# Kernel optimization log

Hardware: AMD Instinct MI355X
Metric: run time of the kernel (lower is better)

## Reference

```python
import jax, jax.numpy as jnp
import numpy as np

D, H, DK, DFF = 256, 8, 32, 1024
EPS = 1e-5

def _layernorm(x, g, b):
    mu = jnp.mean(x, axis=-1, keepdims=True)
    var = jnp.mean((x - mu) ** 2, axis=-1, keepdims=True)
    return (x - mu) * jax.lax.rsqrt(var + EPS) * g + b

def setup_inputs() -> dict:
    key = jax.random.key(0)
    ks = jax.random.split(key, 16)
    s = 1.0 / np.sqrt(D)
    sf = 1.0 / np.sqrt(DFF)
    return {
        "src": jax.random.normal(ks[0], (2, 4096, D), jnp.float32),
        "Wq": jax.random.uniform(ks[1], (H, D, DK), jnp.float32, -s, s),
        "bq": jax.random.uniform(ks[2], (H, DK), jnp.float32, -s, s),
        "Wk": jax.random.uniform(ks[3], (H, D, DK), jnp.float32, -s, s),
        "bk": jax.random.uniform(ks[4], (H, DK), jnp.float32, -s, s),
        "Wv": jax.random.uniform(ks[5], (H, D, DK), jnp.float32, -s, s),
        "bv": jax.random.uniform(ks[6], (H, DK), jnp.float32, -s, s),
        "Wo": jax.random.uniform(ks[7], (H * DK, D), jnp.float32, -s, s),
        "bo": jax.random.uniform(ks[8], (D,), jnp.float32, -s, s),
        "ln1_g": jnp.ones((D,), jnp.float32),
        "ln1_b": jnp.zeros((D,), jnp.float32),
        "W1": jax.random.uniform(ks[9], (D, DFF), jnp.float32, -s, s),
        "b1": jax.random.uniform(ks[10], (DFF,), jnp.float32, -s, s),
        "W2": jax.random.uniform(ks[11], (DFF, D), jnp.float32, -sf, sf),
        "b2": jax.random.uniform(ks[12], (D,), jnp.float32, -sf, sf),
        "ln2_g": jnp.ones((D,), jnp.float32),
        "ln2_b": jnp.zeros((D,), jnp.float32),
    }

def reference(src, Wq, bq, Wk, bk, Wv, bv, Wo, bo, ln1_g, ln1_b, W1, b1, W2, b2, ln2_g, ln2_b):
    B, S, _ = src.shape
    # per-head projections, batched over heads: [B,H,S,DK]
    q = jnp.einsum("bsd,hdk->bhsk", src, Wq) + bq[None, :, None, :]
    k = jnp.einsum("bsd,hdk->bhsk", src, Wk) + bk[None, :, None, :]
    v = jnp.einsum("bsd,hdk->bhsk", src, Wv) + bv[None, :, None, :]
    scale = jnp.sqrt(jnp.asarray(DK, src.dtype))
    scores = jnp.einsum("bhsk,bhtk->bhst", q, k) / scale  # [B,H,S,S]
    attn = jax.nn.softmax(scores, axis=-1)
    ctx = jnp.einsum("bhst,bhtv->bhsv", attn, v)  # [B,H,S,DK]
    ctx = ctx.transpose(0, 2, 1, 3).reshape(B, S, H * DK)  # concat heads
    attn_out = ctx @ Wo + bo
    x = _layernorm(src + attn_out, ln1_g, ln1_b)  # post-LN residual (dropout=0)
    ffn = jnp.maximum(x @ W1 + b1, 0.0) @ W2 + b2
    return _layernorm(x + ffn, ln2_g, ln2_b)
```

## Files before the change

### kernel.cpp

```cpp
#include <hip/hip_runtime.h>
#include <hip/hip_bf16.h>

#define BB   2
#define SS   4096
#define DD   256
#define HH   8
#define DKK  32
#define DFFC 1024
#define BS   (BB*SS)
#define MB   (1024*1024)

#define SCALE2 (0.17677669529663689f * 1.4426950408889634f)

typedef float f32x4 __attribute__((ext_vector_type(4)));
typedef __bf16 bf16x8 __attribute__((ext_vector_type(8)));

static __device__ __forceinline__ unsigned int cvtpk2(float lo, float hi) {
    unsigned int r;
    asm("v_cvt_pk_bf16_f32 %0, %1, %2" : "=v"(r) : "v"(lo), "v"(hi));
    return r;
}
static __device__ __forceinline__ unsigned short f2bf(float f) {
    return (unsigned short)cvtpk2(f, 0.0f);
}

__global__ __launch_bounds__(256) void convert_k(
    const float* __restrict__ src,
    const float* __restrict__ Wq, const float* __restrict__ Wk,
    const float* __restrict__ Wv, const float* __restrict__ Wo,
    const float* __restrict__ W1, const float* __restrict__ W2,
    const float* __restrict__ bq, const float* __restrict__ bk,
    const float* __restrict__ bv,
    unsigned short* __restrict__ srcb, unsigned short* __restrict__ Wqkv_t,
    unsigned short* __restrict__ Wo_t, unsigned short* __restrict__ W1_t,
    unsigned short* __restrict__ W2_t, float* __restrict__ bqkv)
{
    int idx = blockIdx.x * 256 + threadIdx.x;
    if (idx < 2097152) { srcb[idx] = f2bf(src[idx]); return; }
    int i = idx - 2097152;
    if (i < 196608) {
        const int c = i >> 8, d = i & 255;
        const int which = c >> 8, h = (c >> 5) & 7, kk = c & 31;
        const float* W = which == 0 ? Wq : which == 1 ? Wk : Wv;
        Wqkv_t[i] = f2bf(W[h * 8192 + d * 32 + kk]);
        return;
    }
    i -= 196608;
    if (i < 65536) {
        const int n = i >> 8, k2 = i & 255;
        Wo_t[i] = f2bf(Wo[k2 * 256 + n]);
        return;
    }
    i -= 65536;
    if (i < 262144) {
        const int n = i >> 8, k2 = i & 255;
        W1_t[i] = f2bf(W1[k2 * 1024 + n]);
        return;
    }
    i -= 262144;
    if (i < 262144) {
        const int n = i >> 10, k2 = i & 1023;
        W2_t[i] = f2bf(W2[k2 * 256 + n]);
        return;
    }
    i -= 262144;
    if (i < 768)
        bqkv[i] = (i < 256) ? bq[i] : (i < 512) ? bk[i - 256] : bv[i - 512];
}

#define LDA 36

template <int EPI, int K, int BM>
__global__ __launch_bounds__(256) void mfma_gemm_k(
    const unsigned short* __restrict__ A,
    const unsigned short* __restrict__ Bt,
    const float* __restrict__ bias,
    const float* __restrict__ Rres,
    void* __restrict__ Cout, int N)
{
    constexpr int MI = BM / 32;
    __shared__ unsigned short Al[BM * LDA];
    __shared__ unsigned short Bl[64 * LDA];

    const int tid  = threadIdx.x;
    const int w    = tid >> 6, lane = tid & 63;
    const int lq   = lane & 15, lk = lane >> 4;
    const int wr   = w >> 1,   wc = w & 1;
    const int m0   = blockIdx.y * BM, n0 = blockIdx.x * 64;

    const int arow = (BM == 128) ? (tid >> 1) : (tid >> 2);
    const int ac   = (BM == 128) ? ((tid & 1) * 16) : ((tid & 3) * 8);
    const int brow = tid >> 2, bc = (tid & 3) * 8;
    const unsigned short* Ap = A  + (size_t)(m0 + arow) * K + ac;
    const unsigned short* Bp = Bt + (size_t)(n0 + brow) * K + bc;

    f32x4 acc[MI][2];
#pragma unroll
    for (int mi = 0; mi < MI; ++mi)
#pragma unroll
        for (int ni = 0; ni < 2; ++ni) acc[mi][ni] = (f32x4){0.f, 0.f, 0.f, 0.f};

    int4 a0, a1, b0;
    a0 = *(const int4*)(Ap);
    if constexpr (BM == 128) a1 = *(const int4*)(Ap + 8);
    b0 = *(const int4*)(Bp);

    for (int k0 = 0; k0 < K; k0 += 32) {
        __syncthreads();
        *(int4*)&Al[arow * LDA + ac] = a0;
        if constexpr (BM == 128) *(int4*)&Al[arow * LDA + ac + 8] = a1;
        *(int4*)&Bl[brow * LDA + bc] = b0;
        __syncthreads();
        if (k0 + 32 < K) {
            a0 = *(const int4*)(Ap + k0 + 32);
            if constexpr (BM == 128) a1 = *(const int4*)(Ap + k0 + 40);
            b0 = *(const int4*)(Bp + k0 + 32);
        }

        bf16x8 bfrag[2];
#pragma unroll
        for (int ni = 0; ni < 2; ++ni)
            bfrag[ni] = *(const bf16x8*)&Bl[(wc * 32 + ni * 16 + lq) * LDA + lk * 8];
#pragma unroll
        for (int mi = 0; mi < MI; ++mi) {
            const bf16x8 afrag =
                *(const bf16x8*)&Al[(wr * (BM / 2) + mi * 16 + lq) * LDA + lk * 8];
#pragma unroll
            for (int ni = 0; ni < 2; ++ni)
                acc[mi][ni] = __builtin_amdgcn_mfma_f32_16x16x32_bf16(
                    afrag, bfrag[ni], acc[mi][ni], 0, 0, 0);
        }
    }

#pragma unroll
    for (int ni = 0; ni < 2; ++ni) {
        const int col = n0 + wc * 32 + ni * 16 + lq;
        const float bv_ = bias[col];
#pragma unroll
        for (int mi = 0; mi < MI; ++mi) {
#pragma unroll
            for (int r = 0; r < 4; ++r) {
                const int row = m0 + wr * (BM / 2) + mi * 16 + lk * 4 + r;
                float val = acc[mi][ni][r] + bv_;
                if constexpr (EPI == 0) {
                    ((float*)Cout)[(size_t)row * N + col] =
                        val + Rres[(size_t)row * N + col];
                } else if constexpr (EPI == 1) {
                    ((unsigned short*)Cout)[(size_t)row * N + col] =
                        f2bf(fmaxf(val, 0.f));
                } else {
                    const int which = col >> 8, h = (col >> 5) & 7, kk = col & 31;
                    if (which == 0) val *= SCALE2;
                    const int b = row >> 12, s = row & (SS - 1);
                    ((unsigned short*)Cout)[(size_t)which * 2097152 +
                        ((size_t)(b * 8 + h) * SS + s) * 32 + kk] = f2bf(val);
                }
            }
        }
    }
}

#define KVB 128
#define RK  40
#define RVT 136
#define RVP 136

__global__ __launch_bounds__(256) void attn_mfma_k(
    const unsigned short* __restrict__ qb, const unsigned short* __restrict__ kb,
    const unsigned short* __restrict__ vb, unsigned short* __restrict__ ctxb)
{
    __shared__ unsigned short Kl[KVB * RK];
    __shared__ unsigned short Vt[32 * RVT];
    __shared__ unsigned short Pl[4][16 * RVP];

    const int tid  = threadIdx.x;
    const int w    = tid >> 6;
    const int lane = tid & 63;
    const int lq   = lane & 15;
    const int lk   = lane >> 4;
    const int bh   = blockIdx.x;
    const int b    = bh >> 3;
    const int h    = bh & 7;
    const int q0   = blockIdx.y * 64;

    const int rho  = tid >> 1, ksel = tid & 1;
    const int kgt  = ((rho & 15) << 3) | (rho >> 4);
    const int vt   = tid & 127, vh = (tid >> 7) * 16;

    const unsigned short* kg = kb + (size_t)bh * SS * DKK;
    const unsigned short* vg = vb + (size_t)bh * SS * DKK;

    union U16 { int4 i; bf16x8 b; unsigned short s[8]; };

    U16 uq;
    uq.i = *(const int4*)(qb + ((size_t)bh * SS + q0 + w * 16 + lq) * DKK + lk * 8);
    const bf16x8 aq = uq.b;

    float m_[4], l_[4];
    f32x4 o0 = {0.f, 0.f, 0.f, 0.f};
    f32x4 o1 = {0.f, 0.f, 0.f, 0.f};
#pragma unroll
    for (int r = 0; r < 4; ++r) { m_[r] = -INFINITY; l_[r] = 0.f; }

    int4 ka0 = *(const int4*)(kg + (size_t)kgt * DKK + ksel * 16);
    int4 ka1 = *(const int4*)(kg + (size_t)kgt * DKK + ksel * 16 + 8);
    int4 va0 = *(const int4*)(vg + (size_t)vt * DKK + vh);
    int4 va1 = *(const int4*)(vg + (size_t)vt * DKK + vh + 8);

    for (int t0 = 0; t0 < SS; t0 += KVB) {
        __syncthreads();
        *(int4*)&Kl[rho * RK + ksel * 16]     = ka0;
        *(int4*)&Kl[rho * RK + ksel * 16 + 8] = ka1;
        U16 u0, u1; u0.i = va0; u1.i = va1;
#pragma unroll
        for (int j = 0; j < 8; ++j) {
            Vt[(vh + j) * RVT + vt]     = u0.s[j];
            Vt[(vh + 8 + j) * RVT + vt] = u1.s[j];
        }
        __syncthreads();

        if (t0 + KVB < SS) {
            const unsigned short* kn = kg + (size_t)(t0 + KVB) * DKK;
            const unsigned short* vn = vg + (size_t)(t0 + KVB) * DKK;
            ka0 = *(const int4*)(kn + (size_t)kgt * DKK + ksel * 16);
            ka1 = *(const int4*)(kn + (size_t)kgt * DKK + ksel * 16 + 8);
            va0 = *(const int4*)(vn + (size_t)vt * DKK + vh);
            va1 = *(const int4*)(vn + (size_t)vt * DKK + vh + 8);
        }

        f32x4 acc[8];
#pragma unroll
        for (int g = 0; g < 8; ++g) {
            const bf16x8 bk_ = *(const bf16x8*)&Kl[(g * 16 + lq) * RK + lk * 8];
            acc[g] = __builtin_amdgcn_mfma_f32_16x16x32_bf16(
                aq, bk_, (f32x4){0.f, 0.f, 0.f, 0.f}, 0, 0, 0);
        }

        float rm[4];
#pragma unroll
        for (int r = 0; r < 4; ++r) {
            float v = acc[0][r];
#pragma unroll
            for (int g = 1; g < 8; ++g) v = fmaxf(v, acc[g][r]);
            v = fmaxf(v, __shfl_xor(v, 1));
            v = fmaxf(v, __shfl_xor(v, 2));
            v = fmaxf(v, __shfl_xor(v, 4));
            v = fmaxf(v, __shfl_xor(v, 8));
            rm[r] = v;
        }
        const bool grow = (rm[0] > m_[0] + 8.f) || (rm[1] > m_[1] + 8.f) ||
                          (rm[2] > m_[2] + 8.f) || (rm[3] > m_[3] + 8.f);
        if (__any(grow)) {
#pragma unroll
            for (int r = 0; r < 4; ++r) {
                const float mn = fmaxf(m_[r], rm[r]);
                const float c  = exp2f(m_[r] - mn);
                m_[r] = mn;
                l_[r] *= c;
                o0[r] *= c;
                o1[r] *= c;
            }
        }
#pragma unroll
        for (int r = 0; r < 4; ++r) {
            float p[8];
            float s = 0.f;
#pragma unroll
            for (int g = 0; g < 8; ++g) {
                p[g] = exp2f(acc[g][r] - m_[r]);
                s += p[g];
            }
            l_[r] += s;
            int4 pi;
            pi.x = (int)cvtpk2(p[0], p[1]);
            pi.y = (int)cvtpk2(p[2], p[3]);
            pi.z = (int)cvtpk2(p[4], p[5]);
            pi.w = (int)cvtpk2(p[6], p[7]);
            *(int4*)&Pl[w][(lk * 4 + r) * RVP + lq * 8] = pi;
        }

#pragma unroll
        for (int c2 = 0; c2 < 4; ++c2) {
            const bf16x8 pa = *(const bf16x8*)&Pl[w][lq * RVP + c2 * 32 + lk * 8];
            const bf16x8 v0 = *(const bf16x8*)&Vt[lq * RVT + c2 * 32 + lk * 8];
            o0 = __builtin_amdgcn_mfma_f32_16x16x32_bf16(pa, v0, o0, 0, 0, 0);
            const bf16x8 v1 = *(const bf16x8*)&Vt[(16 + lq) * RVT + c2 * 32 + lk * 8];
            o1 = __builtin_amdgcn_mfma_f32_16x16x32_bf16(pa, v1, o1, 0, 0, 0);
        }
    }

#pragma unroll
    for (int r = 0; r < 4; ++r) {
        float ls = l_[r];
        ls += __shfl_xor(ls, 1);
        ls += __shfl_xor(ls, 2);
        ls += __shfl_xor(ls, 4);
        ls += __shfl_xor(ls, 8);
        const float inv = 1.0f / ls;
        const size_t row = (size_t)b * SS + q0 + w * 16 + lk * 4 + r;
        unsigned short* cp = ctxb + row * (HH * DKK) + h * DKK;
        cp[lq]      = f2bf(o0[r] * inv);
        cp[16 + lq] = f2bf(o1[r] * inv);
    }
}

__global__ __launch_bounds__(256) void ln_k(
    const float* __restrict__ y, const float* __restrict__ g,
    const float* __restrict__ be, float* __restrict__ out,
    unsigned short* __restrict__ outb)
{
    const int tid = threadIdx.x;
    const size_t r = blockIdx.x;
    const float val = y[r * DD + tid];
    float s1 = val, s2 = val * val;
#pragma unroll
    for (int i = 1; i < 64; i <<= 1) {
        s1 += __shfl_xor(s1, i, 64);
        s2 += __shfl_xor(s2, i, 64);
    }
    __shared__ float ps1[4], ps2[4];
    const int w = tid >> 6, lane = tid & 63;
    if (lane == 0) { ps1[w] = s1; ps2[w] = s2; }
    __syncthreads();
    const float t1 = ps1[0] + ps1[1] + ps1[2] + ps1[3];
    const float t2 = ps2[0] + ps2[1] + ps2[2] + ps2[3];
    const float mean = t1 * (1.f / DD);
    const float var  = t2 * (1.f / DD) - mean * mean;
    const float rs   = rsqrtf(var + 1e-5f);
    const float res  = (val - mean) * rs * g[tid] + be[tid];
    out[r * DD + tid] = res;
    if (outb) outb[r * DD + tid] = f2bf(res);
}

extern "C" void kernel_launch(void* const* d_in, const int* in_sizes, int n_in,
                              void* d_out, int out_size, void* d_ws, size_t ws_size,
                              hipStream_t stream)
{
    const float* src  = (const float*)d_in[0];
    const float* Wq   = (const float*)d_in[1];
    const float* bq   = (const float*)d_in[2];
    const float* Wk   = (const float*)d_in[3];
    const float* bk   = (const float*)d_in[4];
    const float* Wv   = (const float*)d_in[5];
    const float* bv   = (const float*)d_in[6];
    const float* Wo   = (const float*)d_in[7];
    const float* bo   = (const float*)d_in[8];
    const float* ln1g = (const float*)d_in[9];
    const float* ln1b = (const float*)d_in[10];
    const float* W1   = (const float*)d_in[11];
    const float* b1   = (const float*)d_in[12];
    const float* W2   = (const float*)d_in[13];
    const float* b2   = (const float*)d_in[14];
    const float* ln2g = (const float*)d_in[15];
    const float* ln2b = (const float*)d_in[16];
    float* out = (float*)d_out;

    char* wsb = (char*)d_ws;
    float*          x     = (float*)(wsb);
    unsigned short* xb    = (unsigned short*)(wsb + (size_t) 8 * MB);
    unsigned short* srcb  = (unsigned short*)(wsb + (size_t)12 * MB);
    unsigned short* qb    = (unsigned short*)(wsb + (size_t)16 * MB);
    unsigned short* kb2   = (unsigned short*)(wsb + (size_t)20 * MB);
    unsigned short* vb2   = (unsigned short*)(wsb + (size_t)24 * MB);
    unsigned short* ctxb  = (unsigned short*)(wsb + (size_t)28 * MB);
    float*          y1    = (float*)(wsb + (size_t)32 * MB);
    unsigned short* hh    = (unsigned short*)(wsb + (size_t)12 * MB);
    unsigned short* Wqkv_t= (unsigned short*)(wsb + (size_t)40 * MB);
    unsigned short* Wo_t  = (unsigned short*)(wsb + (size_t)40 * MB + 384 * 1024);
    unsigned short* W1_t  = (unsigned short*)(wsb + (size_t)40 * MB + 512 * 1024);
    unsigned short* W2_t  = (unsigned short*)(wsb + (size_t)40 * MB + 1024 * 1024);
    float*          bqkv  = (float*)(wsb + (size_t)40 * MB + 1536 * 1024);

    convert_k<<<11267, 256, 0, stream>>>(src, Wq, Wk, Wv, Wo, W1, W2, bq, bk, bv,
                                         srcb, Wqkv_t, Wo_t, W1_t, W2_t, bqkv);

    mfma_gemm_k<2, DD, 128><<<dim3(12, 64), 256, 0, stream>>>(
        srcb, Wqkv_t, bqkv, nullptr, qb, 768);

    attn_mfma_k<<<dim3(BB * HH, SS / 64), 256, 0, stream>>>(qb, kb2, vb2, ctxb);

    mfma_gemm_k<0, DD, 64><<<dim3(4, 128), 256, 0, stream>>>(
        ctxb, Wo_t, bo, src, y1, DD);

    ln_k<<<BS, DD, 0, stream>>>(y1, ln1g, ln1b, x, xb);

    mfma_gemm_k<1, DD, 128><<<dim3(16, 64), 256, 0, stream>>>(
        xb, W1_t, b1, nullptr, hh, DFFC);

    mfma_gemm_k<0, DFFC, 64><<<dim3(4, 128), 256, 0, stream>>>(
        hh, W2_t, b2, x, out, DD);

    ln_k<<<BS, DD, 0, stream>>>(out, ln2g, ln2b, out, nullptr);
}
```

Before: 284.6 us.

## Fuse src conversion into QKV GEMM, pre-transpose V, MFMA row sums, K64 tiles

The fp32 src is now converted to bf16 inside a dedicated QKV GEMM, so the separate conversion pass and its intermediate buffer go away. A new kernel writes V pre-transposed, which turns the scalar transposing LDS stores in attention into vector stores. The softmax row sums are now accumulated with an extra MFMA against a ones vector instead of scalar adds and shuffle reductions. The generic GEMM K-step is also widened to 64 to halve the number of barriers. The trade-offs are an extra kernel launch with its own memory traffic for the transpose, and row sums taken from bf16-rounded probabilities.

New measurement: 354.7 us. 24.6% more time.

```diff
diff --git a/kernel.cpp b/kernel.cpp
--- a/kernel.cpp
+++ b/kernel.cpp
@@ -25,19 +25,16 @@
 }
 
 __global__ __launch_bounds__(256) void convert_k(
-    const float* __restrict__ src,
     const float* __restrict__ Wq, const float* __restrict__ Wk,
     const float* __restrict__ Wv, const float* __restrict__ Wo,
     const float* __restrict__ W1, const float* __restrict__ W2,
     const float* __restrict__ bq, const float* __restrict__ bk,
     const float* __restrict__ bv,
-    unsigned short* __restrict__ srcb, unsigned short* __restrict__ Wqkv_t,
-    unsigned short* __restrict__ Wo_t, unsigned short* __restrict__ W1_t,
-    unsigned short* __restrict__ W2_t, float* __restrict__ bqkv)
-{
-    int idx = blockIdx.x * 256 + threadIdx.x;
-    if (idx < 2097152) { srcb[idx] = f2bf(src[idx]); return; }
-    int i = idx - 2097152;
+    unsigned short* __restrict__ Wqkv_t, unsigned short* __restrict__ Wo_t,
+    unsigned short* __restrict__ W1_t, unsigned short* __restrict__ W2_t,
+    float* __restrict__ bqkv)
+{
+    int i = blockIdx.x * 256 + threadIdx.x;
     if (i < 196608) {
         const int c = i >> 8, d = i & 255;
         const int which = c >> 8, h = (c >> 5) & 7, kk = c & 31;
@@ -47,20 +44,17 @@
     }
     i -= 196608;
     if (i < 65536) {
-        const int n = i >> 8, k2 = i & 255;
-        Wo_t[i] = f2bf(Wo[k2 * 256 + n]);
+        Wo_t[i] = f2bf(Wo[(i & 255) * 256 + (i >> 8)]);
         return;
     }
     i -= 65536;
     if (i < 262144) {
-        const int n = i >> 8, k2 = i & 255;
-        W1_t[i] = f2bf(W1[k2 * 1024 + n]);
+        W1_t[i] = f2bf(W1[(i & 255) * 1024 + (i >> 8)]);
         return;
     }
     i -= 262144;
     if (i < 262144) {
-        const int n = i >> 10, k2 = i & 1023;
-        W2_t[i] = f2bf(W2[k2 * 256 + n]);
+        W2_t[i] = f2bf(W2[(i & 1023) * 256 + (i >> 10)]);
         return;
     }
     i -= 262144;
@@ -69,6 +63,90 @@
 }
 
 #define LDA 36
+
+__global__ __launch_bounds__(256) void qkv_gemm_k(
+    const float* __restrict__ A, const unsigned short* __restrict__ Bt,
+    const float* __restrict__ bias, unsigned short* __restrict__ Cout)
+{
+    __shared__ unsigned short Al[128 * LDA];
+    __shared__ unsigned short Bl[64 * LDA];
+
+    const int tid  = threadIdx.x;
+    const int w    = tid >> 6, lane = tid & 63;
+    const int lq   = lane & 15, lk = lane >> 4;
+    const int wr   = w >> 1,   wc = w & 1;
+    const int m0   = blockIdx.y * 128, n0 = blockIdx.x * 64;
+
+    const int arow = tid >> 1, ac = (tid & 1) * 16;
+    const int brow = tid >> 2, bc = (tid & 3) * 8;
+    const float* Ap = A + (size_t)(m0 + arow) * DD + ac;
+    const unsigned short* Bp = Bt + (size_t)(n0 + brow) * DD + bc;
+
+    f32x4 acc[4][2];
+#pragma unroll
+    for (int mi = 0; mi < 4; ++mi)
+#pragma unroll
+        for (int ni = 0; ni < 2; ++ni) acc[mi][ni] = (f32x4){0.f, 0.f, 0.f, 0.f};
+
+    float4 f[4];
+    int4 b0;
+#pragma unroll
+    for (int i = 0; i < 4; ++i) f[i] = *(const float4*)(Ap + i * 4);
+    b0 = *(const int4*)(Bp);
+
+    for (int k0 = 0; k0 < DD; k0 += 32) {
+        int4 aA, aB;
+        aA.x = (int)cvtpk2(f[0].x, f[0].y); aA.y = (int)cvtpk2(f[0].z, f[0].w);
+        aA.z = (int)cvtpk2(f[1].x, f[1].y); aA.w = (int)cvtpk2(f[1].z, f[1].w);
+        aB.x = (int)cvtpk2(f[2].x, f[2].y); aB.y = (int)cvtpk2(f[2].z, f[2].w);
+        aB.z = (int)cvtpk2(f[3].x, f[3].y); aB.w = (int)cvtpk2(f[3].z, f[3].w);
+        __syncthreads();
+        *(int4*)&Al[arow * LDA + ac]     = aA;
+        *(int4*)&Al[arow * LDA + ac + 8] = aB;
+        *(int4*)&Bl[brow * LDA + bc]     = b0;
+        __syncthreads();
+        if (k0 + 32 < DD) {
+#pragma unroll
+            for (int i = 0; i < 4; ++i) f[i] = *(const float4*)(Ap + k0 + 32 + i * 4);
+            b0 = *(const int4*)(Bp + k0 + 32);
+        }
+
+        bf16x8 bfrag[2];
+#pragma unroll
+        for (int ni = 0; ni < 2; ++ni)
+            bfrag[ni] = *(const bf16x8*)&Bl[(wc * 32 + ni * 16 + lq) * LDA + lk * 8];
+#pragma unroll
+        for (int mi = 0; mi < 4; ++mi) {
+            const bf16x8 afrag =
+                *(const bf16x8*)&Al[(wr * 64 + mi * 16 + lq) * LDA + lk * 8];
+#pragma unroll
+            for (int ni = 0; ni < 2; ++ni)
+                acc[mi][ni] = __builtin_amdgcn_mfma_f32_16x16x32_bf16(
+                    afrag, bfrag[ni], acc[mi][ni], 0, 0, 0);
+        }
+    }
+
+#pragma unroll
+    for (int ni = 0; ni < 2; ++ni) {
+        const int col = n0 + wc * 32 + ni * 16 + lq;
+        const float bv_ = bias[col];
+        const int which = col >> 8, h = (col >> 5) & 7, kk = col & 31;
+#pragma unroll
+        for (int mi = 0; mi < 4; ++mi) {
+#pragma unroll
+            for (int r = 0; r < 4; ++r) {
+                const int row = m0 + wr * 64 + mi * 16 + lk * 4 + r;
+                float val = acc[mi][ni][r] + bv_;
+                if (which == 0) val *= SCALE2;
+                const int b = row >> 12, s = row & (SS - 1);
+                Cout[(size_t)which * 2097152 +
+                     ((size_t)(b * 8 + h) * SS + s) * 32 + kk] = f2bf(val);
+            }
+        }
+    }
+}
+
+#define LDB 72
 
 template <int EPI, int K, int BM>
 __global__ __launch_bounds__(256) void mfma_gemm_k(
@@ -79,8 +157,8 @@
     void* __restrict__ Cout, int N)
 {
     constexpr int MI = BM / 32;
-    __shared__ unsigned short Al[BM * LDA];
-    __shared__ unsigned short Bl[64 * LDA];
+    __shared__ unsigned short Al[BM * LDB];
+    __shared__ unsigned short Bl[64 * LDB];
 
     const int tid  = threadIdx.x;
     const int w    = tid >> 6, lane = tid & 63;
@@ -89,8 +167,8 @@
     const int m0   = blockIdx.y * BM, n0 = blockIdx.x * 64;
 
     const int arow = (BM == 128) ? (tid >> 1) : (tid >> 2);
-    const int ac   = (BM == 128) ? ((tid & 1) * 16) : ((tid & 3) * 8);
-    const int brow = tid >> 2, bc = (tid & 3) * 8;
+    const int ac   = (BM == 128) ? ((tid & 1) * 32) : ((tid & 3) * 16);
+    const int brow = tid >> 2, bc = (tid & 3) * 16;
     const unsigned short* Ap = A  + (size_t)(m0 + arow) * K + ac;
     const unsigned short* Bp = Bt + (size_t)(n0 + brow) * K + bc;
 
@@ -100,35 +178,43 @@
 #pragma unroll
         for (int ni = 0; ni < 2; ++ni) acc[mi][ni] = (f32x4){0.f, 0.f, 0.f, 0.f};
 
-    int4 a0, a1, b0;
-    a0 = *(const int4*)(Ap);
-    if constexpr (BM == 128) a1 = *(const int4*)(Ap + 8);
-    b0 = *(const int4*)(Bp);
-
-    for (int k0 = 0; k0 < K; k0 += 32) {
-        __syncthreads();
-        *(int4*)&Al[arow * LDA + ac] = a0;
-        if constexpr (BM == 128) *(int4*)&Al[arow * LDA + ac + 8] = a1;
-        *(int4*)&Bl[brow * LDA + bc] = b0;
-        __syncthreads();
-        if (k0 + 32 < K) {
-            a0 = *(const int4*)(Ap + k0 + 32);
-            if constexpr (BM == 128) a1 = *(const int4*)(Ap + k0 + 40);
-            b0 = *(const int4*)(Bp + k0 + 32);
-        }
-
-        bf16x8 bfrag[2];
-#pragma unroll
-        for (int ni = 0; ni < 2; ++ni)
-            bfrag[ni] = *(const bf16x8*)&Bl[(wc * 32 + ni * 16 + lq) * LDA + lk * 8];
-#pragma unroll
-        for (int mi = 0; mi < MI; ++mi) {
-            const bf16x8 afrag =
-                *(const bf16x8*)&Al[(wr * (BM / 2) + mi * 16 + lq) * LDA + lk * 8];
+    constexpr int NA = (BM == 128) ? 4 : 2;
+    int4 a[NA], b[2];
+#pragma unroll
+    for (int i = 0; i < NA; ++i) a[i] = *(const int4*)(Ap + i * 8);
+    b[0] = *(const int4*)(Bp);
+    b[1] = *(const int4*)(Bp + 8);
+
+    for (int k0 = 0; k0 < K; k0 += 64) {
+        __syncthreads();
+#pragma unroll
+        for (int i = 0; i < NA; ++i) *(int4*)&Al[arow * LDB + ac + i * 8] = a[i];
+        *(int4*)&Bl[brow * LDB + bc]     = b[0];
+        *(int4*)&Bl[brow * LDB + bc + 8] = b[1];
+        __syncthreads();
+        if (k0 + 64 < K) {
+#pragma unroll
+            for (int i = 0; i < NA; ++i) a[i] = *(const int4*)(Ap + k0 + 64 + i * 8);
+            b[0] = *(const int4*)(Bp + k0 + 64);
+            b[1] = *(const int4*)(Bp + k0 + 72);
+        }
+
+#pragma unroll
+        for (int k2 = 0; k2 < 2; ++k2) {
+            bf16x8 bfrag[2];
 #pragma unroll
             for (int ni = 0; ni < 2; ++ni)
-                acc[mi][ni] = __builtin_amdgcn_mfma_f32_16x16x32_bf16(
-                    afrag, bfrag[ni], acc[mi][ni], 0, 0, 0);
+                bfrag[ni] = *(const bf16x8*)
+                    &Bl[(wc * 32 + ni * 16 + lq) * LDB + k2 * 32 + lk * 8];
+#pragma unroll
+            for (int mi = 0; mi < MI; ++mi) {
+                const bf16x8 afrag = *(const bf16x8*)
+                    &Al[(wr * (BM / 2) + mi * 16 + lq) * LDB + k2 * 32 + lk * 8];
+#pragma unroll
+                for (int ni = 0; ni < 2; ++ni)
+                    acc[mi][ni] = __builtin_amdgcn_mfma_f32_16x16x32_bf16(
+                        afrag, bfrag[ni], acc[mi][ni], 0, 0, 0);
+            }
         }
     }
 
@@ -145,19 +231,28 @@
                 if constexpr (EPI == 0) {
                     ((float*)Cout)[(size_t)row * N + col] =
                         val + Rres[(size_t)row * N + col];
-                } else if constexpr (EPI == 1) {
+                } else {
                     ((unsigned short*)Cout)[(size_t)row * N + col] =
                         f2bf(fmaxf(val, 0.f));
-                } else {
-                    const int which = col >> 8, h = (col >> 5) & 7, kk = col & 31;
-                    if (which == 0) val *= SCALE2;
-                    const int b = row >> 12, s = row & (SS - 1);
-                    ((unsigned short*)Cout)[(size_t)which * 2097152 +
-                        ((size_t)(b * 8 + h) * SS + s) * 32 + kk] = f2bf(val);
                 }
             }
         }
     }
+}
+
+__global__ __launch_bounds__(256) void vT_k(
+    const unsigned short* __restrict__ vb, unsigned short* __restrict__ vbT)
+{
+    const int tid = threadIdx.x;
+    const int bh  = blockIdx.x >> 6;
+    const int s0  = (blockIdx.x & 63) * 64;
+    const int kk  = tid >> 3;
+    const int sp  = (tid & 7) * 8;
+    const unsigned short* src = vb + ((size_t)bh * SS + s0 + sp) * DKK + kk;
+    union { int4 i; unsigned short s[8]; } u;
+#pragma unroll
+    for (int j = 0; j < 8; ++j) u.s[j] = src[(size_t)j * DKK];
+    *(int4*)(vbT + ((size_t)bh * DKK + kk) * SS + s0 + sp) = u.i;
 }
 
 #define KVB 128
@@ -167,7 +262,7 @@
 
 __global__ __launch_bounds__(256) void attn_mfma_k(
     const unsigned short* __restrict__ qb, const unsigned short* __restrict__ kb,
-    const unsigned short* __restrict__ vb, unsigned short* __restrict__ ctxb)
+    const unsigned short* __restrict__ vbT, unsigned short* __restrict__ ctxb)
 {
     __shared__ unsigned short Kl[KVB * RK];
     __shared__ unsigned short Vt[32 * RVT];
@@ -185,10 +280,10 @@
 
     const int rho  = tid >> 1, ksel = tid & 1;
     const int kgt  = ((rho & 15) << 3) | (rho >> 4);
-    const int vt   = tid & 127, vh = (tid >> 7) * 16;
-
-    const unsigned short* kg = kb + (size_t)bh * SS * DKK;
-    const unsigned short* vg = vb + (size_t)bh * SS * DKK;
+    const int vdv  = tid >> 3, vsp = (tid & 7) * 16;
+
+    const unsigned short* kg  = kb  + (size_t)bh * SS * DKK;
+    const unsigned short* vtg = vbT + ((size_t)bh * DKK + vdv) * SS + vsp;
 
     union U16 { int4 i; bf16x8 b; unsigned short s[8]; };
 
@@ -196,36 +291,35 @@
     uq.i = *(const int4*)(qb + ((size_t)bh * SS + q0 + w * 16 + lq) * DKK + lk * 8);
     const bf16x8 aq = uq.b;
 
-    float m_[4], l_[4];
-    f32x4 o0 = {0.f, 0.f, 0.f, 0.f};
-    f32x4 o1 = {0.f, 0.f, 0.f, 0.f};
-#pragma unroll
-    for (int r = 0; r < 4; ++r) { m_[r] = -INFINITY; l_[r] = 0.f; }
+    const int4 onesi = make_int4(0x3F803F80, 0x3F803F80, 0x3F803F80, 0x3F803F80);
+    const bf16x8 onesb = *(const bf16x8*)&onesi;
+
+    float m_[4];
+    f32x4 o0   = {0.f, 0.f, 0.f, 0.f};
+    f32x4 o1   = {0.f, 0.f, 0.f, 0.f};
+    f32x4 lacc = {0.f, 0.f, 0.f, 0.f};
+#pragma unroll
+    for (int r = 0; r < 4; ++r) m_[r] = -INFINITY;
 
     int4 ka0 = *(const int4*)(kg + (size_t)kgt * DKK + ksel * 16);
     int4 ka1 = *(const int4*)(kg + (size_t)kgt * DKK + ksel * 16 + 8);
-    int4 va0 = *(const int4*)(vg + (size_t)vt * DKK + vh);
-    int4 va1 = *(const int4*)(vg + (size_t)vt * DKK + vh + 8);
+    int4 va0 = *(const int4*)(vtg);
+    int4 va1 = *(const int4*)(vtg + 8);
 
     for (int t0 = 0; t0 < SS; t0 += KVB) {
         __syncthreads();
         *(int4*)&Kl[rho * RK + ksel * 16]     = ka0;
         *(int4*)&Kl[rho * RK + ksel * 16 + 8] = ka1;
-        U16 u0, u1; u0.i = va0; u1.i = va1;
-#pragma unroll
-        for (int j = 0; j < 8; ++j) {
-            Vt[(vh + j) * RVT + vt]     = u0.s[j];
-            Vt[(vh + 8 + j) * RVT + vt] = u1.s[j];
-        }
+        *(int4*)&Vt[vdv * RVT + vsp]          = va0;
+        *(int4*)&Vt[vdv * RVT + vsp + 8]      = va1;
         __syncthreads();
 
         if (t0 + KVB < SS) {
             const unsigned short* kn = kg + (size_t)(t0 + KVB) * DKK;
-            const unsigned short* vn = vg + (size_t)(t0 + KVB) * DKK;
             ka0 = *(const int4*)(kn + (size_t)kgt * DKK + ksel * 16);
             ka1 = *(const int4*)(kn + (size_t)kgt * DKK + ksel * 16 + 8);
-            va0 = *(const int4*)(vn + (size_t)vt * DKK + vh);
-            va1 = *(const int4*)(vn + (size_t)vt * DKK + vh + 8);
+            va0 = *(const int4*)(vtg + t0 + KVB);
+            va1 = *(const int4*)(vtg + t0 + KVB + 8);
         }
 
         f32x4 acc[8];
@@ -256,7 +350,7 @@
                 const float mn = fmaxf(m_[r], rm[r]);
                 const float c  = exp2f(m_[r] - mn);
                 m_[r] = mn;
-                l_[r] *= c;
+                lacc[r] *= c;
                 o0[r] *= c;
                 o1[r] *= c;
             }
@@ -264,13 +358,8 @@
 #pragma unroll
         for (int r = 0; r < 4; ++r) {
             float p[8];
-            float s = 0.f;
-#pragma unroll
-            for (int g = 0; g < 8; ++g) {
-                p[g] = exp2f(acc[g][r] - m_[r]);
-                s += p[g];
-            }
-            l_[r] += s;
+#pragma unroll
+            for (int g = 0; g < 8; ++g) p[g] = exp2f(acc[g][r] - m_[r]);
             int4 pi;
             pi.x = (int)cvtpk2(p[0], p[1]);
             pi.y = (int)cvtpk2(p[2], p[3]);
@@ -282,6 +371,7 @@
 #pragma unroll
         for (int c2 = 0; c2 < 4; ++c2) {
             const bf16x8 pa = *(const bf16x8*)&Pl[w][lq * RVP + c2 * 32 + lk * 8];
+            lacc = __builtin_amdgcn_mfma_f32_16x16x32_bf16(pa, onesb, lacc, 0, 0, 0);
             const bf16x8 v0 = *(const bf16x8*)&Vt[lq * RVT + c2 * 32 + lk * 8];
             o0 = __builtin_amdgcn_mfma_f32_16x16x32_bf16(pa, v0, o0, 0, 0, 0);
             const bf16x8 v1 = *(const bf16x8*)&Vt[(16 + lq) * RVT + c2 * 32 + lk * 8];
@@ -291,12 +381,7 @@
 
 #pragma unroll
     for (int r = 0; r < 4; ++r) {
-        float ls = l_[r];
-        ls += __shfl_xor(ls, 1);
-        ls += __shfl_xor(ls, 2);
-        ls += __shfl_xor(ls, 4);
-        ls += __shfl_xor(ls, 8);
-        const float inv = 1.0f / ls;
+        const float inv = 1.0f / lacc[r];
         const size_t row = (size_t)b * SS + q0 + w * 16 + lk * 4 + r;
         unsigned short* cp = ctxb + row * (HH * DKK) + h * DKK;
         cp[lq]      = f2bf(o0[r] * inv);
@@ -358,10 +443,10 @@
     char* wsb = (char*)d_ws;
     float*          x     = (float*)(wsb);
     unsigned short* xb    = (unsigned short*)(wsb + (size_t) 8 * MB);
-    unsigned short* srcb  = (unsigned short*)(wsb + (size_t)12 * MB);
-    unsigned short* qb    = (unsigned short*)(wsb + (size_t)16 * MB);
-    unsigned short* kb2   = (unsigned short*)(wsb + (size_t)20 * MB);
-    unsigned short* vb2   = (unsigned short*)(wsb + (size_t)24 * MB);
+    unsigned short* qb    = (unsigned short*)(wsb + (size_t)12 * MB);
+    unsigned short* kb2   = (unsigned short*)(wsb + (size_t)16 * MB);
+    unsigned short* vb2   = (unsigned short*)(wsb + (size_t)20 * MB);
+    unsigned short* vbT   = (unsigned short*)(wsb + (size_t)24 * MB);
     unsigned short* ctxb  = (unsigned short*)(wsb + (size_t)28 * MB);
     float*          y1    = (float*)(wsb + (size_t)32 * MB);
     unsigned short* hh    = (unsigned short*)(wsb + (size_t)12 * MB);
@@ -371,13 +456,14 @@
     unsigned short* W2_t  = (unsigned short*)(wsb + (size_t)40 * MB + 1024 * 1024);
     float*          bqkv  = (float*)(wsb + (size_t)40 * MB + 1536 * 1024);
 
-    convert_k<<<11267, 256, 0, stream>>>(src, Wq, Wk, Wv, Wo, W1, W2, bq, bk, bv,
-                                         srcb, Wqkv_t, Wo_t, W1_t, W2_t, bqkv);
-
-    mfma_gemm_k<2, DD, 128><<<dim3(12, 64), 256, 0, stream>>>(
-        srcb, Wqkv_t, bqkv, nullptr, qb, 768);
-
-    attn_mfma_k<<<dim3(BB * HH, SS / 64), 256, 0, stream>>>(qb, kb2, vb2, ctxb);
+    convert_k<<<3075, 256, 0, stream>>>(Wq, Wk, Wv, Wo, W1, W2, bq, bk, bv,
+                                        Wqkv_t, Wo_t, W1_t, W2_t, bqkv);
+
+    qkv_gemm_k<<<dim3(12, 64), 256, 0, stream>>>(src, Wqkv_t, bqkv, qb);
+
+    vT_k<<<1024, 256, 0, stream>>>(vb2, vbT);
+
+    attn_mfma_k<<<dim3(BB * HH, SS / 64), 256, 0, stream>>>(qb, kb2, vbT, ctxb);
 
     mfma_gemm_k<0, DD, 64><<<dim3(4, 128), 256, 0, stream>>>(
         ctxb, Wo_t, bo, src, y1, DD);
```
